# Performance work log

Hardware: AMD Instinct MI355X
Metric: run time of the kernel (lower is better)

The kernel has to match this reference:

```python
import jax, jax.numpy as jnp
import numpy as np
import math

B, T, C, H = 4, 1024, 1024, 16
D = C // H
EPS = 1e-5


def layer_norm(x, w, b):
    mu = jnp.mean(x, axis=-1, keepdims=True)
    var = jnp.mean(jnp.square(x - mu), axis=-1, keepdims=True)
    return (x - mu) * jax.lax.rsqrt(var + EPS) * w + b


def setup_inputs() -> dict:
    key = jax.random.key(0)
    ks = jax.random.split(key, 8)
    s = 0.02
    return {
        "x": jax.random.normal(ks[0], (B, T, C), jnp.float32),
        "attention_mask": jnp.ones((B, T), jnp.float32),
        "ln1_w": jnp.ones((C,), jnp.float32),
        "ln1_b": jnp.zeros((C,), jnp.float32),
        "w_attn": jax.random.normal(ks[1], (C, 3 * C), jnp.float32) * s,
        "b_attn": jnp.zeros((3 * C,), jnp.float32),
        "w_proj": jax.random.normal(ks[2], (C, C), jnp.float32) * s,
        "b_proj": jnp.zeros((C,), jnp.float32),
        "threshold": jnp.float32(0.0005),  # (layer_idx+1)/n_layer * final_token_threshold
        "ln2_w": jnp.ones((C,), jnp.float32),
        "ln2_b": jnp.zeros((C,), jnp.float32),
        "w_fc": jax.random.normal(ks[3], (C, 4 * C), jnp.float32) * s,
        "b_fc": jnp.zeros((4 * C,), jnp.float32),
        "w_fc2": jax.random.normal(ks[4], (4 * C, C), jnp.float32) * s,
        "b_fc2": jnp.zeros((C,), jnp.float32),
    }


def reference(x, attention_mask, ln1_w, ln1_b, w_attn, b_attn, w_proj, b_proj,
              threshold, ln2_w, ln2_b, w_fc, b_fc, w_fc2, b_fc2):
    # ---- attention (eval mode, dropout=0; hard masking_mode) ----
    h = layer_norm(x, ln1_w, ln1_b)
    qkv = h @ w_attn + b_attn                      # (B,T,3C)
    q, k, v = jnp.split(qkv, 3, axis=-1)
    q = q.reshape(B, T, H, D).transpose(0, 2, 1, 3)  # (B,H,T,D)
    k = k.reshape(B, T, H, D).transpose(0, 2, 1, 3)
    v = v.reshape(B, T, H, D).transpose(0, 2, 1, 3)

    scale = 1.0 / math.sqrt(D)
    logits = jnp.einsum("bhqd,bhkd->bhqk", q, k) * scale  # (B,H,T,T)
    causal = jnp.tril(jnp.ones((T, T), bool))
    neg_inf = jnp.float32(-jnp.inf)
    logits = jnp.where(causal[None, None], logits, neg_inf)
    # key-side validity mask (applied in original's manual pass; mask is all-ones
    # here so flash-path y == softmax(causal logits) @ v as well)
    logits = jnp.where(attention_mask[:, None, None, :] == 0, neg_inf, logits)
    att = jax.nn.softmax(logits, axis=-1)

    y = jnp.einsum("bhqk,bhkd->bhqd", att, v)      # (B,H,T,D)
    importance = att.mean(axis=1).mean(axis=1)     # (B,T): mean over heads, then queries

    y = y.transpose(0, 2, 1, 3).reshape(B, T, C)
    x = x + (y @ w_proj + b_proj)

    # ---- hard pruning mask ----
    pruning_mask = (importance >= threshold).astype(x.dtype)
    combined_mask = attention_mask * pruning_mask
    x = x * combined_mask[:, :, None]

    # ---- MLP ----
    h2 = layer_norm(x, ln2_w, ln2_b)
    f = jax.nn.gelu(h2 @ w_fc + b_fc, approximate=False)
    x = x + (f @ w_fc2 + b_fc2)

    pruning_loss = jnp.float32(0.0)  # hard mode -> always 0
    return (x, combined_mask, pruning_loss)
```

## Files before the change

kernel.cpp:

```cpp
#include <hip/hip_runtime.h>
#include <cstdint>
#include <cstring>

typedef unsigned short u16;
typedef short bf16x8 __attribute__((ext_vector_type(8)));
typedef float f32x4 __attribute__((ext_vector_type(4)));

#define MFMA16(a,b,c) __builtin_amdgcn_mfma_f32_16x16x32_bf16(a,b,c,0,0,0)


__device__ __forceinline__ u16 f2bf(float f) {
  union { float f; uint32_t u; } un; un.f = f;
  uint32_t u = un.u;
  u += 0x7FFFu + ((u >> 16) & 1u);
  return (u16)(u >> 16);
}

__device__ __forceinline__ float bf2f(u16 h) {
  union { uint32_t u; float f; } un; un.u = ((uint32_t)h) << 16;
  return un.f;
}

__device__ __forceinline__ float gelu_fast(float v) {
  float u = 0.7978845608028654f * (v + 0.044715f * v * v * v);
  float e = __expf(2.f * u);
  float th = 1.f - __fdividef(2.f, e + 1.f);
  return 0.5f * v * (1.f + th);
}

__device__ __forceinline__ void gl_lds16(const void* g, void* l) {
  __builtin_amdgcn_global_load_lds(
      (__attribute__((address_space(1))) void*)(const_cast<void*>(g)),
      (__attribute__((address_space(3))) void*)l, 16, 0, 0);
}


__global__ __launch_bounds__(256) void transpose_all(
    const float* __restrict__ wa, const float* __restrict__ wp,
    const float* __restrict__ wf, const float* __restrict__ wf2,
    u16* __restrict__ wat, u16* __restrict__ wpt,
    u16* __restrict__ wft, u16* __restrict__ wf2t)
{
  __shared__ float tile[32][33];
  int id = blockIdx.x;
  const float* W; u16* Wt; int K, N, bx, by;
  if (id < 3072)      { W = wa;  Wt = wat;  K = 1024; N = 3072; bx = id % 96;  by = id / 96; }
  else if (id < 4096) { id -= 3072; W = wp;  Wt = wpt;  K = 1024; N = 1024; bx = id % 32; by = id / 32; }
  else if (id < 8192) { id -= 4096; W = wf;  Wt = wft;  K = 1024; N = 4096; bx = id % 128; by = id / 128; }
  else                { id -= 8192; W = wf2; Wt = wf2t; K = 4096; N = 1024; bx = id % 32; by = id / 32; }
  int kt = by * 32, nt = bx * 32;
  int tx = threadIdx.x, ty = threadIdx.y;
#pragma unroll
  for (int i = 0; i < 4; ++i)
    tile[ty + i * 8][tx] = W[(size_t)(kt + ty + i * 8) * N + nt + tx];
  __syncthreads();
#pragma unroll
  for (int i = 0; i < 4; ++i)
    Wt[(size_t)(nt + ty + i * 8) * K + kt + tx] = f2bf(tile[tx][ty + i * 8]);
}


__global__ __launch_bounds__(256) void ln_bf16(
    const float* __restrict__ x, const float* __restrict__ wt,
    const float* __restrict__ bs, u16* __restrict__ out)
{
  int row = blockIdx.x;
  int tid = threadIdx.x, lane = tid & 63, w = tid >> 6;
  const float* xr = x + (size_t)row * 1024;
  float4 v = *(const float4*)(xr + tid * 4);
  float s = v.x + v.y + v.z + v.w;
  float sq = v.x * v.x + v.y * v.y + v.z * v.z + v.w * v.w;
#pragma unroll
  for (int o = 1; o < 64; o <<= 1) { s += __shfl_xor(s, o); sq += __shfl_xor(sq, o); }
  __shared__ float ls[4], lq[4];
  if (lane == 0) { ls[w] = s; lq[w] = sq; }
  __syncthreads();
  s = ls[0] + ls[1] + ls[2] + ls[3];
  sq = lq[0] + lq[1] + lq[2] + lq[3];
  float mu = s * (1.f / 1024.f);
  float var = sq * (1.f / 1024.f) - mu * mu;
  float rstd = rsqrtf(var + 1e-5f);
  float4 wv = *(const float4*)(wt + tid * 4);
  float4 bv = *(const float4*)(bs + tid * 4);
  ushort4 o4;
  o4.x = f2bf((v.x - mu) * rstd * wv.x + bv.x);
  o4.y = f2bf((v.y - mu) * rstd * wv.y + bv.y);
  o4.z = f2bf((v.z - mu) * rstd * wv.z + bv.z);
  o4.w = f2bf((v.w - mu) * rstd * wv.w + bv.w);
  *(ushort4*)(out + (size_t)row * 1024 + tid * 4) = o4;
}


__device__ __forceinline__ void gemm_mainloop_db(
    const u16* __restrict__ Abase, const u16* __restrict__ Bbase,
    int lda, int ldb, int nIter, f32x4 acc[4][4])
{
  __shared__ __align__(16) u16 lA[2][128 * 32];
  __shared__ __align__(16) u16 lB[2][128 * 32];

  const int tid = threadIdx.x;
  const int lane = tid & 63;
  const int w = tid >> 6;
  const int wr = (w >> 1) * 64;
  const int wc = (w & 1) * 64;
  const int laneM = lane & 15;
  const int q4 = lane >> 4;

#pragma unroll
  for (int i = 0; i < 4; ++i)
#pragma unroll
    for (int j = 0; j < 4; ++j)
      acc[i][j] = f32x4{0.f, 0.f, 0.f, 0.f};

  const int off0 = w * 1024 + lane * 16;
  const int off1 = off0 + 4096;
  const int rA0 = off0 >> 6;
  const int rA1 = off1 >> 6;
  const int scb = (((lane & 3) ^ ((lane >> 3) & 3)) << 4);

  const size_t sA = (size_t)lda * 2;
  const size_t sB = (size_t)ldb * 2;
  const char* pA0 = (const char*)Abase + (size_t)rA0 * sA + scb;
  const char* pA1 = (const char*)Abase + (size_t)rA1 * sA + scb;
  const char* pB0 = (const char*)Bbase + (size_t)rA0 * sB + scb;
  const char* pB1 = (const char*)Bbase + (size_t)rA1 * sB + scb;
  char* dA0 = (char*)&lA[0][0] + off0;
  char* dA1 = (char*)&lA[0][0] + off1;
  char* dB0 = (char*)&lB[0][0] + off0;
  char* dB1 = (char*)&lB[0][0] + off1;

  gl_lds16(pA0, dA0); gl_lds16(pA1, dA1);
  gl_lds16(pB0, dB0); gl_lds16(pB1, dB1);
  pA0 += 64; pA1 += 64; pB0 += 64; pB1 += 64;
  __syncthreads();

  const int rdswz = ((q4 ^ ((laneM >> 1) & 3)) << 4);

  for (int it = 0; it < nIter; ++it) {
    const int cur = it & 1;
    const int nb = cur ^ 1;
    if (it + 1 < nIter) {
      gl_lds16(pA0, dA0 + nb * 8192);
      gl_lds16(pA1, dA1 + nb * 8192);
      gl_lds16(pB0, dB0 + nb * 8192);
      gl_lds16(pB1, dB1 + nb * 8192);
      pA0 += 64; pA1 += 64; pB0 += 64; pB1 += 64;
    }
    const char* aRd = (const char*)&lA[cur][0] + (wr + laneM) * 64 + rdswz;
    const char* bRd = (const char*)&lB[cur][0] + (wc + laneM) * 64 + rdswz;
    bf16x8 af[4], bfr[4];
#pragma unroll
    for (int t = 0; t < 4; ++t) {
      af[t]  = *(const bf16x8*)(aRd + t * 1024);
      bfr[t] = *(const bf16x8*)(bRd + t * 1024);
    }
#pragma unroll
    for (int i = 0; i < 4; ++i)
#pragma unroll
      for (int j = 0; j < 4; ++j)
        acc[i][j] = MFMA16(af[i], bfr[j], acc[i][j]);
    if (it + 1 < nIter) __syncthreads();
  }
}


__global__ __launch_bounds__(256, 4) void gemm_qkv(
    const u16* __restrict__ A, const u16* __restrict__ Bt,
    const float* __restrict__ bias,
    u16* __restrict__ qo, u16* __restrict__ ko, u16* __restrict__ vo)
{
  f32x4 acc[4][4];
  int m0 = blockIdx.y * 128, n0 = blockIdx.x * 128;
  gemm_mainloop_db(A + (size_t)m0 * 1024, Bt + (size_t)n0 * 1024, 1024, 1024, 32, acc);
  const int lane = threadIdx.x & 63, w = threadIdx.x >> 6;
  const int wr = (w >> 1) * 64, wc = (w & 1) * 64;
  const int laneM = lane & 15, q4 = lane >> 4;
  const int which = (n0 >> 10);
#pragma unroll
  for (int ti = 0; ti < 4; ++ti) {
#pragma unroll
    for (int tj = 0; tj < 4; ++tj) {
      int n = n0 + wc + tj * 16 + laneM;
      int c = n & 1023;
      int hh = c >> 6, d = c & 63;
      float bval = bias[n];
      if (which == 2) {
        int m0r = m0 + wr + ti * 16 + q4 * 4;
        int b = m0r >> 10, t0 = m0r & 1023;
        ushort4 o4;
        o4.x = f2bf(acc[ti][tj][0] + bval);
        o4.y = f2bf(acc[ti][tj][1] + bval);
        o4.z = f2bf(acc[ti][tj][2] + bval);
        o4.w = f2bf(acc[ti][tj][3] + bval);
        *(ushort4*)&vo[((size_t)((b * 16 + hh) * 64 + d)) * 1024 + t0] = o4;
      } else {
        u16* dst = (which == 0) ? qo : ko;
#pragma unroll
        for (int r = 0; r < 4; ++r) {
          int m = m0 + wr + ti * 16 + q4 * 4 + r;
          int b = m >> 10, t = m & 1023;
          dst[((size_t)((b * 16 + hh) * 1024 + t)) * 64 + d] = f2bf(acc[ti][tj][r] + bval);
        }
      }
    }
  }
}

__global__ __launch_bounds__(256, 4) void gemm_proj(
    const u16* __restrict__ A, const u16* __restrict__ Bt,
    const float* __restrict__ bias, const float* __restrict__ xin,
    const float* __restrict__ maskv, float* __restrict__ x2)
{
  f32x4 acc[4][4];
  int m0 = blockIdx.y * 128, n0 = blockIdx.x * 128;
  gemm_mainloop_db(A + (size_t)m0 * 1024, Bt + (size_t)n0 * 1024, 1024, 1024, 32, acc);
  const int lane = threadIdx.x & 63, w = threadIdx.x >> 6;
  const int wr = (w >> 1) * 64, wc = (w & 1) * 64;
  const int laneM = lane & 15, q4 = lane >> 4;
#pragma unroll
  for (int ti = 0; ti < 4; ++ti) {
#pragma unroll
    for (int tj = 0; tj < 4; ++tj) {
      int n = n0 + wc + tj * 16 + laneM;
      float bval = bias[n];
#pragma unroll
      for (int r = 0; r < 4; ++r) {
        int m = m0 + wr + ti * 16 + q4 * 4 + r;
        float v = xin[(size_t)m * 1024 + n] + acc[ti][tj][r] + bval;
        x2[(size_t)m * 1024 + n] = v * maskv[m];
      }
    }
  }
}

__global__ __launch_bounds__(256, 4) void gemm_fc(
    const u16* __restrict__ A, const u16* __restrict__ Bt,
    const float* __restrict__ bias, u16* __restrict__ fo)
{
  f32x4 acc[4][4];
  int m0 = blockIdx.y * 128, n0 = blockIdx.x * 128;
  gemm_mainloop_db(A + (size_t)m0 * 1024, Bt + (size_t)n0 * 1024, 1024, 1024, 32, acc);
  const int lane = threadIdx.x & 63, w = threadIdx.x >> 6;
  const int wr = (w >> 1) * 64, wc = (w & 1) * 64;
  const int laneM = lane & 15, q4 = lane >> 4;
#pragma unroll
  for (int ti = 0; ti < 4; ++ti) {
#pragma unroll
    for (int tj = 0; tj < 4; ++tj) {
      int n = n0 + wc + tj * 16 + laneM;
      float bval = bias[n];
#pragma unroll
      for (int r = 0; r < 4; ++r) {
        int m = m0 + wr + ti * 16 + q4 * 4 + r;
        fo[(size_t)m * 4096 + n] = f2bf(gelu_fast(acc[ti][tj][r] + bval));
      }
    }
  }
}

__global__ __launch_bounds__(256, 4) void gemm_fc2_splitk(
    const u16* __restrict__ A, const u16* __restrict__ Bt,
    u16* __restrict__ pall)
{
  int id = blockIdx.x;
  int r = id & 7, j = id >> 3;
  int mt = r * 4 + (j >> 5);
  int rem = j & 31;
  int n0 = (rem & 7) * 128;
  int kz = rem >> 3;
  int m0 = mt * 128;
  f32x4 acc[4][4];
  gemm_mainloop_db(A + (size_t)m0 * 4096 + kz * 1024,
                   Bt + (size_t)n0 * 4096 + kz * 1024, 4096, 4096, 32, acc);
  u16* p = pall + (size_t)kz * 4096 * 1024;
  const int lane = threadIdx.x & 63, w = threadIdx.x >> 6;
  const int wr = (w >> 1) * 64, wc = (w & 1) * 64;
  const int laneM = lane & 15, q4 = lane >> 4;
#pragma unroll
  for (int ti = 0; ti < 4; ++ti) {
#pragma unroll
    for (int tj = 0; tj < 4; ++tj) {
      int n = n0 + wc + tj * 16 + laneM;
#pragma unroll
      for (int r2 = 0; r2 < 4; ++r2) {
        int m = m0 + wr + ti * 16 + q4 * 4 + r2;
        p[(size_t)m * 1024 + n] = f2bf(acc[ti][tj][r2]);
      }
    }
  }
}

__global__ __launch_bounds__(256) void fc2_finalize(
    const float* __restrict__ x2, const float* __restrict__ bias,
    const u16* __restrict__ pall, float* __restrict__ out)
{
  int i = blockIdx.x * 256 + threadIdx.x;
  int col4 = i & 255;
  float4 a = ((const float4*)x2)[i];
  float4 b = ((const float4*)bias)[col4];
  float s0 = a.x + b.x, s1 = a.y + b.y, s2 = a.z + b.z, s3 = a.w + b.w;
#pragma unroll
  for (int z = 0; z < 4; ++z) {
    ushort4 u = ((const ushort4*)(pall + (size_t)z * 4194304))[i];
    s0 += bf2f(u.x); s1 += bf2f(u.y); s2 += bf2f(u.z); s3 += bf2f(u.w);
  }
  float4 o; o.x = s0; o.y = s1; o.z = s2; o.w = s3;
  ((float4*)out)[i] = o;
}


__global__ __launch_bounds__(512) void attn_fwd(
    const u16* __restrict__ qb, const u16* __restrict__ kb, const u16* __restrict__ vtb,
    u16* __restrict__ yb, float* __restrict__ part)
{
  const int id = blockIdx.x;
  const int slot = (id & 7) ^ ((id >> 8) & 1);
  const int qbi = (slot & 1) ? (slot >> 1) : (7 - (slot >> 1));
  const int bh = id >> 3;
  const int b = bh >> 4, h = bh & 15;

  const int tid = threadIdx.x, lane = tid & 63, w = tid >> 6;
  const int q0 = qbi * 128;
  const int laneM = lane & 15, q4 = lane >> 4;
  const float scale = 0.125f;

  __shared__ __align__(16) u16 lK[2][64 * 72];
  __shared__ __align__(16) u16 lV[2][64 * 72];
  __shared__ __align__(16) u16 lP[8][16 * 72];
  __shared__ float part_s[1024];

  part_s[tid] = 0.f;
  part_s[tid + 512] = 0.f;

  bf16x8 qf[2];
  {
    const u16* qrow = qb + ((size_t)(bh * 1024 + q0 + w * 16 + laneM)) * 64 + q4 * 8;
    qf[0] = *(const bf16x8*)qrow;
    qf[1] = *(const bf16x8*)(qrow + 32);
  }

  const int nkt = 2 * qbi + 2;
  const int srow = tid >> 3;
  const int scol = (tid & 7) * 8;
  const u16* kbase = kb + (size_t)bh * 65536;
  const u16* vbase = vtb + (size_t)bh * 65536;

  float lrow[4] = {0.f, 0.f, 0.f, 0.f};
  {
    uint4 pk = *(const uint4*)(kbase + (size_t)srow * 64 + scol);
    *(uint4*)&lK[0][srow * 72 + scol] = pk;
    __syncthreads();
    for (int kt = 0; kt < nkt; ++kt) {
      const int cur = kt & 1;
      if (kt + 1 < nkt)
        pk = *(const uint4*)(kbase + (size_t)((kt + 1) * 64 + srow) * 64 + scol);
#pragma unroll
      for (int tj = 0; tj < 4; ++tj) {
        const u16* kp = &lK[cur][(tj * 16 + laneM) * 72 + q4 * 8];
        bf16x8 k0 = *(const bf16x8*)kp;
        bf16x8 k1 = *(const bf16x8*)(kp + 32);
        f32x4 z = {0.f, 0.f, 0.f, 0.f};
        z = MFMA16(qf[0], k0, z);
        z = MFMA16(qf[1], k1, z);
        int kc = kt * 64 + tj * 16 + laneM;
#pragma unroll
        for (int r = 0; r < 4; ++r) {
          int qg = q0 + w * 16 + q4 * 4 + r;
          lrow[r] += (kc <= qg) ? __expf(z[r] * scale) : 0.f;
        }
      }
      if (kt + 1 < nkt) *(uint4*)&lK[cur ^ 1][srow * 72 + scol] = pk;
      __syncthreads();
    }
  }
  float linv[4];
#pragma unroll
  for (int r = 0; r < 4; ++r) {
    float s = lrow[r];
    s += __shfl_xor(s, 1); s += __shfl_xor(s, 2);
    s += __shfl_xor(s, 4); s += __shfl_xor(s, 8);
    linv[r] = 1.f / s;
  }

  f32x4 o_[4];
#pragma unroll
  for (int dt = 0; dt < 4; ++dt) o_[dt] = f32x4{0.f, 0.f, 0.f, 0.f};

  {
    uint4 pk = *(const uint4*)(kbase + (size_t)srow * 64 + scol);
    uint4 pv = *(const uint4*)(vbase + (size_t)srow * 1024 + scol);
    *(uint4*)&lK[0][srow * 72 + scol] = pk;
    *(uint4*)&lV[0][srow * 72 + scol] = pv;
    __syncthreads();
    for (int kt = 0; kt < nkt; ++kt) {
      const int cur = kt & 1;
      if (kt + 1 < nkt) {
        pk = *(const uint4*)(kbase + (size_t)((kt + 1) * 64 + srow) * 64 + scol);
        pv = *(const uint4*)(vbase + (size_t)srow * 1024 + (kt + 1) * 64 + scol);
      }
      u16* lPw = &lP[w][0];
#pragma unroll
      for (int tj = 0; tj < 4; ++tj) {
        const u16* kp = &lK[cur][(tj * 16 + laneM) * 72 + q4 * 8];
        bf16x8 k0 = *(const bf16x8*)kp;
        bf16x8 k1 = *(const bf16x8*)(kp + 32);
        f32x4 z = {0.f, 0.f, 0.f, 0.f};
        z = MFMA16(qf[0], k0, z);
        z = MFMA16(qf[1], k1, z);
        int kc = kt * 64 + tj * 16 + laneM;
        float cs = 0.f;
#pragma unroll
        for (int r = 0; r < 4; ++r) {
          int qg = q0 + w * 16 + q4 * 4 + r;
          float pvf = (kc <= qg) ? __expf(z[r] * scale) * linv[r] : 0.f;
          cs += pvf;
          lPw[(q4 * 4 + r) * 72 + tj * 16 + laneM] = f2bf(pvf);
        }
        cs += __shfl_xor(cs, 16);
        cs += __shfl_xor(cs, 32);
        if (lane < 16) atomicAdd(&part_s[kt * 64 + tj * 16 + lane], cs);
      }
#pragma unroll
      for (int ss = 0; ss < 2; ++ss) {
        bf16x8 pf = *(const bf16x8*)&lP[w][laneM * 72 + ss * 32 + q4 * 8];
#pragma unroll
        for (int dt = 0; dt < 4; ++dt) {
          bf16x8 vf = *(const bf16x8*)&lV[cur][(dt * 16 + laneM) * 72 + ss * 32 + q4 * 8];
          o_[dt] = MFMA16(pf, vf, o_[dt]);
        }
      }
      if (kt + 1 < nkt) {
        *(uint4*)&lK[cur ^ 1][srow * 72 + scol] = pk;
        *(uint4*)&lV[cur ^ 1][srow * 72 + scol] = pv;
      }
      __syncthreads();
    }
  }

  const int kmax = nkt * 64;
  for (int i = tid; i < kmax; i += 512)
    atomicAdd(&part[(size_t)bh * 1024 + i], part_s[i]);

#pragma unroll
  for (int dt = 0; dt < 4; ++dt)
#pragma unroll
    for (int r = 0; r < 4; ++r) {
      int qg = q0 + w * 16 + q4 * 4 + r;
      yb[((size_t)(b * 1024 + qg)) * 1024 + h * 64 + dt * 16 + laneM] = f2bf(o_[dt][r]);
    }
}


__global__ __launch_bounds__(256) void finalize_mask(
    const float* __restrict__ part, const float* __restrict__ amask,
    const float* __restrict__ thr, float* __restrict__ mask_ws,
    float* __restrict__ out_mask, float* __restrict__ out_loss)
{
  int i = blockIdx.x * 256 + threadIdx.x;
  if (i >= 4096) return;
  int b = i >> 10;
  int t = i & 1023;
  float s = 0.f;
#pragma unroll
  for (int hh = 0; hh < 16; ++hh) s += part[(size_t)(b * 16 + hh) * 1024 + t];
  float imp = s * (1.0f / 16384.0f);
  float mv = (imp >= thr[0]) ? amask[i] : 0.f;
  mask_ws[i] = mv;
  out_mask[i] = mv;
  if (i == 0) out_loss[0] = 0.f;
}


extern "C" void kernel_launch(void* const* d_in, const int* in_sizes, int n_in,
                              void* d_out, int out_size, void* d_ws, size_t ws_size,
                              hipStream_t stream) {
  const float* x      = (const float*)d_in[0];
  const float* amask  = (const float*)d_in[1];
  const float* ln1w   = (const float*)d_in[2];
  const float* ln1b   = (const float*)d_in[3];
  const float* w_attn = (const float*)d_in[4];
  const float* b_attn = (const float*)d_in[5];
  const float* w_proj = (const float*)d_in[6];
  const float* b_proj = (const float*)d_in[7];
  const float* thr    = (const float*)d_in[8];
  const float* ln2w   = (const float*)d_in[9];
  const float* ln2b   = (const float*)d_in[10];
  const float* w_fc   = (const float*)d_in[11];
  const float* b_fc   = (const float*)d_in[12];
  const float* w_fc2  = (const float*)d_in[13];
  const float* b_fc2  = (const float*)d_in[14];
  float* out = (float*)d_out;

  char* ws = (char*)d_ws;
  size_t off = 0;
  auto alloc = [&](size_t bytes) -> char* {
    char* p = ws + off;
    off += (bytes + 255) & ~(size_t)255;
    return p;
  };
  u16* wattnT = (u16*)alloc((size_t)3072 * 1024 * 2);
  u16* wprojT = (u16*)alloc((size_t)1024 * 1024 * 2);
  u16* wfcT   = (u16*)alloc((size_t)4096 * 1024 * 2);
  u16* wfc2T  = (u16*)alloc((size_t)1024 * 4096 * 2);
  u16* hbuf   = (u16*)alloc((size_t)4096 * 1024 * 2);
  u16* qbuf   = (u16*)alloc((size_t)64 * 1024 * 64 * 2);
  u16* kbuf   = (u16*)alloc((size_t)64 * 1024 * 64 * 2);
  u16* vtbuf  = (u16*)alloc((size_t)64 * 64 * 1024 * 2);
  u16* ybuf   = (u16*)alloc((size_t)4096 * 1024 * 2);
  float* part = (float*)alloc((size_t)64 * 1024 * 4);
  float* maskws = (float*)alloc((size_t)4096 * 4);
  float* x2   = (float*)alloc((size_t)4096 * 1024 * 4);
  u16* h2     = (u16*)alloc((size_t)4096 * 1024 * 2);
  u16* fbuf   = (u16*)alloc((size_t)4096 * 4096 * 2);

  u16* pall = qbuf;

  transpose_all<<<12288, dim3(32, 8), 0, stream>>>(
      w_attn, w_proj, w_fc, w_fc2, wattnT, wprojT, wfcT, wfc2T);

  hipMemsetAsync(part, 0, (size_t)64 * 1024 * 4, stream);

  ln_bf16<<<4096, 256, 0, stream>>>(x, ln1w, ln1b, hbuf);

  gemm_qkv<<<dim3(24, 32), 256, 0, stream>>>(hbuf, wattnT, b_attn, qbuf, kbuf, vtbuf);

  attn_fwd<<<512, 512, 0, stream>>>(qbuf, kbuf, vtbuf, ybuf, part);

  finalize_mask<<<16, 256, 0, stream>>>(part, amask, thr, maskws,
                                        out + 4194304, out + 4198400);

  gemm_proj<<<dim3(8, 32), 256, 0, stream>>>(ybuf, wprojT, b_proj, x, maskws, x2);

  ln_bf16<<<4096, 256, 0, stream>>>(x2, ln2w, ln2b, h2);

  gemm_fc<<<dim3(32, 32), 256, 0, stream>>>(h2, wfcT, b_fc, fbuf);

  gemm_fc2_splitk<<<1024, 256, 0, stream>>>(fbuf, wfc2T, pall);

  fc2_finalize<<<4096, 256, 0, stream>>>(x2, b_fc2, pall, out);
}
```

Before: 347.1 us.

## Fuse prep, mask finalize, and split-K reduction into neighbouring kernels

Weight transposes and the first LayerNorm now run in one `prep` launch, which also zeroes the split-K tile counters. Attention blocks store their importance partials per query block with plain stores instead of atomics, so the memset of `part` goes away. `gemm_proj` now sums those partials itself to build the pruning mask, removing the `finalize_mask` kernel. The split-K FC2 reduction moves into the last-arriving block per tile via an atomic counter, removing `fc2_finalize`. The aim is fewer launches and less contention on atomics. In exchange, `part` needs eight times more scratch, and each proj block redundantly reads 128 partial values per row.

```diff
diff --git a/kernel.cpp b/kernel.cpp
--- a/kernel.cpp
+++ b/kernel.cpp
@@ -35,28 +35,61 @@
 }
 
 
-__global__ __launch_bounds__(256) void transpose_all(
+__global__ __launch_bounds__(256) void prep(
     const float* __restrict__ wa, const float* __restrict__ wp,
     const float* __restrict__ wf, const float* __restrict__ wf2,
     u16* __restrict__ wat, u16* __restrict__ wpt,
-    u16* __restrict__ wft, u16* __restrict__ wf2t)
+    u16* __restrict__ wft, u16* __restrict__ wf2t,
+    const float* __restrict__ x, const float* __restrict__ ln1w,
+    const float* __restrict__ ln1b, u16* __restrict__ hbuf,
+    unsigned* __restrict__ cnt)
 {
   __shared__ float tile[32][33];
+  __shared__ float ls[4], lq[4];
   int id = blockIdx.x;
-  const float* W; u16* Wt; int K, N, bx, by;
-  if (id < 3072)      { W = wa;  Wt = wat;  K = 1024; N = 3072; bx = id % 96;  by = id / 96; }
-  else if (id < 4096) { id -= 3072; W = wp;  Wt = wpt;  K = 1024; N = 1024; bx = id % 32; by = id / 32; }
-  else if (id < 8192) { id -= 4096; W = wf;  Wt = wft;  K = 1024; N = 4096; bx = id % 128; by = id / 128; }
-  else                { id -= 8192; W = wf2; Wt = wf2t; K = 4096; N = 1024; bx = id % 32; by = id / 32; }
-  int kt = by * 32, nt = bx * 32;
-  int tx = threadIdx.x, ty = threadIdx.y;
-#pragma unroll
-  for (int i = 0; i < 4; ++i)
-    tile[ty + i * 8][tx] = W[(size_t)(kt + ty + i * 8) * N + nt + tx];
-  __syncthreads();
-#pragma unroll
-  for (int i = 0; i < 4; ++i)
-    Wt[(size_t)(nt + ty + i * 8) * K + kt + tx] = f2bf(tile[tx][ty + i * 8]);
+  int tid = threadIdx.x;
+  if (blockIdx.x == 0) cnt[tid] = 0u;
+
+  if (id < 12288) {
+    const float* W; u16* Wt; int K, N, bx, by;
+    if (id < 3072)      { W = wa;  Wt = wat;  K = 1024; N = 3072; bx = id % 96;  by = id / 96; }
+    else if (id < 4096) { id -= 3072; W = wp;  Wt = wpt;  K = 1024; N = 1024; bx = id % 32; by = id / 32; }
+    else if (id < 8192) { id -= 4096; W = wf;  Wt = wft;  K = 1024; N = 4096; bx = id % 128; by = id / 128; }
+    else                { id -= 8192; W = wf2; Wt = wf2t; K = 4096; N = 1024; bx = id % 32; by = id / 32; }
+    int kt = by * 32, nt = bx * 32;
+    int tx = tid & 31, ty = tid >> 5;
+#pragma unroll
+    for (int i = 0; i < 4; ++i)
+      tile[ty + i * 8][tx] = W[(size_t)(kt + ty + i * 8) * N + nt + tx];
+    __syncthreads();
+#pragma unroll
+    for (int i = 0; i < 4; ++i)
+      Wt[(size_t)(nt + ty + i * 8) * K + kt + tx] = f2bf(tile[tx][ty + i * 8]);
+  } else {
+    int row = id - 12288;
+    int lane = tid & 63, w = tid >> 6;
+    const float* xr = x + (size_t)row * 1024;
+    float4 v = *(const float4*)(xr + tid * 4);
+    float s = v.x + v.y + v.z + v.w;
+    float sq = v.x * v.x + v.y * v.y + v.z * v.z + v.w * v.w;
+#pragma unroll
+    for (int o = 1; o < 64; o <<= 1) { s += __shfl_xor(s, o); sq += __shfl_xor(sq, o); }
+    if (lane == 0) { ls[w] = s; lq[w] = sq; }
+    __syncthreads();
+    s = ls[0] + ls[1] + ls[2] + ls[3];
+    sq = lq[0] + lq[1] + lq[2] + lq[3];
+    float mu = s * (1.f / 1024.f);
+    float var = sq * (1.f / 1024.f) - mu * mu;
+    float rstd = rsqrtf(var + 1e-5f);
+    float4 wv = *(const float4*)(ln1w + tid * 4);
+    float4 bv = *(const float4*)(ln1b + tid * 4);
+    ushort4 o4;
+    o4.x = f2bf((v.x - mu) * rstd * wv.x + bv.x);
+    o4.y = f2bf((v.y - mu) * rstd * wv.y + bv.y);
+    o4.z = f2bf((v.z - mu) * rstd * wv.z + bv.z);
+    o4.w = f2bf((v.w - mu) * rstd * wv.w + bv.w);
+    *(ushort4*)(hbuf + (size_t)row * 1024 + tid * 4) = o4;
+  }
 }
 
 
@@ -209,7 +242,53 @@
 __global__ __launch_bounds__(256, 4) void gemm_proj(
     const u16* __restrict__ A, const u16* __restrict__ Bt,
     const float* __restrict__ bias, const float* __restrict__ xin,
-    const float* __restrict__ maskv, float* __restrict__ x2)
+    const float* __restrict__ part, const float* __restrict__ amask,
+    const float* __restrict__ thr, float* __restrict__ x2,
+    float* __restrict__ out_mask, float* __restrict__ out_loss)
+{
+  __shared__ float lmask[128];
+  int m0 = blockIdx.y * 128, n0 = blockIdx.x * 128;
+  int tid = threadIdx.x;
+  if (tid < 128) {
+    int m = m0 + tid;
+    int b = m >> 10, t = m & 1023;
+    const float* pb = part + (size_t)(b * 16) * 1024 + t;
+    float s = 0.f;
+#pragma unroll 4
+    for (int qh = 0; qh < 128; ++qh)
+      s += pb[(size_t)((qh >> 4) * 64 + (qh & 15)) * 1024];
+    float imp = s * (1.0f / 16384.0f);
+    float mv = (imp >= thr[0]) ? amask[m] : 0.f;
+    lmask[tid] = mv;
+    if (n0 == 0) out_mask[m] = mv;
+  }
+  if (n0 == 0 && m0 == 0 && tid == 0) out_loss[0] = 0.f;
+
+  f32x4 acc[4][4];
+  gemm_mainloop_db(A + (size_t)m0 * 1024, Bt + (size_t)n0 * 1024, 1024, 1024, 32, acc);
+  const int lane = threadIdx.x & 63, w = threadIdx.x >> 6;
+  const int wr = (w >> 1) * 64, wc = (w & 1) * 64;
+  const int laneM = lane & 15, q4 = lane >> 4;
+#pragma unroll
+  for (int ti = 0; ti < 4; ++ti) {
+#pragma unroll
+    for (int tj = 0; tj < 4; ++tj) {
+      int n = n0 + wc + tj * 16 + laneM;
+      float bval = bias[n];
+#pragma unroll
+      for (int r = 0; r < 4; ++r) {
+        int lm = wr + ti * 16 + q4 * 4 + r;
+        int m = m0 + lm;
+        float v = xin[(size_t)m * 1024 + n] + acc[ti][tj][r] + bval;
+        x2[(size_t)m * 1024 + n] = v * lmask[lm];
+      }
+    }
+  }
+}
+
+__global__ __launch_bounds__(256, 4) void gemm_fc(
+    const u16* __restrict__ A, const u16* __restrict__ Bt,
+    const float* __restrict__ bias, u16* __restrict__ fo)
 {
   f32x4 acc[4][4];
   int m0 = blockIdx.y * 128, n0 = blockIdx.x * 128;
@@ -226,32 +305,6 @@
 #pragma unroll
       for (int r = 0; r < 4; ++r) {
         int m = m0 + wr + ti * 16 + q4 * 4 + r;
-        float v = xin[(size_t)m * 1024 + n] + acc[ti][tj][r] + bval;
-        x2[(size_t)m * 1024 + n] = v * maskv[m];
-      }
-    }
-  }
-}
-
-__global__ __launch_bounds__(256, 4) void gemm_fc(
-    const u16* __restrict__ A, const u16* __restrict__ Bt,
-    const float* __restrict__ bias, u16* __restrict__ fo)
-{
-  f32x4 acc[4][4];
-  int m0 = blockIdx.y * 128, n0 = blockIdx.x * 128;
-  gemm_mainloop_db(A + (size_t)m0 * 1024, Bt + (size_t)n0 * 1024, 1024, 1024, 32, acc);
-  const int lane = threadIdx.x & 63, w = threadIdx.x >> 6;
-  const int wr = (w >> 1) * 64, wc = (w & 1) * 64;
-  const int laneM = lane & 15, q4 = lane >> 4;
-#pragma unroll
-  for (int ti = 0; ti < 4; ++ti) {
-#pragma unroll
-    for (int tj = 0; tj < 4; ++tj) {
-      int n = n0 + wc + tj * 16 + laneM;
-      float bval = bias[n];
-#pragma unroll
-      for (int r = 0; r < 4; ++r) {
-        int m = m0 + wr + ti * 16 + q4 * 4 + r;
         fo[(size_t)m * 4096 + n] = f2bf(gelu_fast(acc[ti][tj][r] + bval));
       }
     }
@@ -260,7 +313,9 @@
 
 __global__ __launch_bounds__(256, 4) void gemm_fc2_splitk(
     const u16* __restrict__ A, const u16* __restrict__ Bt,
-    u16* __restrict__ pall)
+    u16* __restrict__ pall, const float* __restrict__ x2,
+    const float* __restrict__ bias, float* __restrict__ out,
+    unsigned* __restrict__ cnt)
 {
   int id = blockIdx.x;
   int r = id & 7, j = id >> 3;
@@ -273,7 +328,8 @@
   gemm_mainloop_db(A + (size_t)m0 * 4096 + kz * 1024,
                    Bt + (size_t)n0 * 4096 + kz * 1024, 4096, 4096, 32, acc);
   u16* p = pall + (size_t)kz * 4096 * 1024;
-  const int lane = threadIdx.x & 63, w = threadIdx.x >> 6;
+  const int tid = threadIdx.x;
+  const int lane = tid & 63, w = tid >> 6;
   const int wr = (w >> 1) * 64, wc = (w & 1) * 64;
   const int laneM = lane & 15, q4 = lane >> 4;
 #pragma unroll
@@ -288,24 +344,34 @@
       }
     }
   }
-}
-
-__global__ __launch_bounds__(256) void fc2_finalize(
-    const float* __restrict__ x2, const float* __restrict__ bias,
-    const u16* __restrict__ pall, float* __restrict__ out)
-{
-  int i = blockIdx.x * 256 + threadIdx.x;
-  int col4 = i & 255;
-  float4 a = ((const float4*)x2)[i];
-  float4 b = ((const float4*)bias)[col4];
-  float s0 = a.x + b.x, s1 = a.y + b.y, s2 = a.z + b.z, s3 = a.w + b.w;
-#pragma unroll
-  for (int z = 0; z < 4; ++z) {
-    ushort4 u = ((const ushort4*)(pall + (size_t)z * 4194304))[i];
-    s0 += bf2f(u.x); s1 += bf2f(u.y); s2 += bf2f(u.z); s3 += bf2f(u.w);
-  }
-  float4 o; o.x = s0; o.y = s1; o.z = s2; o.w = s3;
-  ((float4*)out)[i] = o;
+
+  __shared__ unsigned done;
+  __syncthreads();
+  const int tile = mt * 8 + (n0 >> 7);
+  if (tid == 0) {
+    __threadfence();
+    done = atomicAdd(&cnt[tile], 1u);
+  }
+  __syncthreads();
+  if (done == 3u) {
+    __threadfence();
+#pragma unroll
+    for (int k = 0; k < 16; ++k) {
+      int idx = k * 256 + tid;
+      int rr = idx >> 5, c = idx & 31;
+      size_t row = (size_t)(m0 + rr);
+      float4 a = ((const float4*)(x2 + row * 1024 + n0))[c];
+      float4 b = ((const float4*)(bias + n0))[c];
+      float s0 = a.x + b.x, s1 = a.y + b.y, s2 = a.z + b.z, s3 = a.w + b.w;
+#pragma unroll
+      for (int z = 0; z < 4; ++z) {
+        ushort4 u = ((const ushort4*)(pall + (size_t)z * 4194304 + row * 1024 + n0))[c];
+        s0 += bf2f(u.x); s1 += bf2f(u.y); s2 += bf2f(u.z); s3 += bf2f(u.w);
+      }
+      float4 o; o.x = s0; o.y = s1; o.z = s2; o.w = s3;
+      ((float4*)(out + row * 1024 + n0))[c] = o;
+    }
+  }
 }
 
 
@@ -437,9 +503,11 @@
     }
   }
 
-  const int kmax = nkt * 64;
-  for (int i = tid; i < kmax; i += 512)
-    atomicAdd(&part[(size_t)bh * 1024 + i], part_s[i]);
+  {
+    float* pd = part + (size_t)(qbi * 64 + bh) * 1024;
+    pd[tid] = part_s[tid];
+    pd[tid + 512] = part_s[tid + 512];
+  }
 
 #pragma unroll
   for (int dt = 0; dt < 4; ++dt)
@@ -448,26 +516,6 @@
       int qg = q0 + w * 16 + q4 * 4 + r;
       yb[((size_t)(b * 1024 + qg)) * 1024 + h * 64 + dt * 16 + laneM] = f2bf(o_[dt][r]);
     }
-}
-
-
-__global__ __launch_bounds__(256) void finalize_mask(
-    const float* __restrict__ part, const float* __restrict__ amask,
-    const float* __restrict__ thr, float* __restrict__ mask_ws,
-    float* __restrict__ out_mask, float* __restrict__ out_loss)
-{
-  int i = blockIdx.x * 256 + threadIdx.x;
-  if (i >= 4096) return;
-  int b = i >> 10;
-  int t = i & 1023;
-  float s = 0.f;
-#pragma unroll
-  for (int hh = 0; hh < 16; ++hh) s += part[(size_t)(b * 16 + hh) * 1024 + t];
-  float imp = s * (1.0f / 16384.0f);
-  float mv = (imp >= thr[0]) ? amask[i] : 0.f;
-  mask_ws[i] = mv;
-  out_mask[i] = mv;
-  if (i == 0) out_loss[0] = 0.f;
 }
 
 
@@ -507,35 +555,28 @@
   u16* kbuf   = (u16*)alloc((size_t)64 * 1024 * 64 * 2);
   u16* vtbuf  = (u16*)alloc((size_t)64 * 64 * 1024 * 2);
   u16* ybuf   = (u16*)alloc((size_t)4096 * 1024 * 2);
-  float* part = (float*)alloc((size_t)64 * 1024 * 4);
-  float* maskws = (float*)alloc((size_t)4096 * 4);
+  float* part = (float*)alloc((size_t)8 * 64 * 1024 * 4);
+  unsigned* cnt = (unsigned*)alloc((size_t)256 * 4);
   float* x2   = (float*)alloc((size_t)4096 * 1024 * 4);
   u16* h2     = (u16*)alloc((size_t)4096 * 1024 * 2);
   u16* fbuf   = (u16*)alloc((size_t)4096 * 4096 * 2);
 
   u16* pall = qbuf;
 
-  transpose_all<<<12288, dim3(32, 8), 0, stream>>>(
-      w_attn, w_proj, w_fc, w_fc2, wattnT, wprojT, wfcT, wfc2T);
-
-  hipMemsetAsync(part, 0, (size_t)64 * 1024 * 4, stream);
-
-  ln_bf16<<<4096, 256, 0, stream>>>(x, ln1w, ln1b, hbuf);
+  prep<<<16384, 256, 0, stream>>>(w_attn, w_proj, w_fc, w_fc2,
+                                  wattnT, wprojT, wfcT, wfc2T,
+                                  x, ln1w, ln1b, hbuf, cnt);
 
   gemm_qkv<<<dim3(24, 32), 256, 0, stream>>>(hbuf, wattnT, b_attn, qbuf, kbuf, vtbuf);
 
   attn_fwd<<<512, 512, 0, stream>>>(qbuf, kbuf, vtbuf, ybuf, part);
 
-  finalize_mask<<<16, 256, 0, stream>>>(part, amask, thr, maskws,
-                                        out + 4194304, out + 4198400);
-
-  gemm_proj<<<dim3(8, 32), 256, 0, stream>>>(ybuf, wprojT, b_proj, x, maskws, x2);
+  gemm_proj<<<dim3(8, 32), 256, 0, stream>>>(ybuf, wprojT, b_proj, x, part, amask,
+                                             thr, x2, out + 4194304, out + 4198400);
 
   ln_bf16<<<4096, 256, 0, stream>>>(x2, ln2w, ln2b, h2);
 
   gemm_fc<<<dim3(32, 32), 256, 0, stream>>>(h2, wfcT, b_fc, fbuf);
 
-  gemm_fc2_splitk<<<1024, 256, 0, stream>>>(fbuf, wfc2T, pall);
-
-  fc2_finalize<<<4096, 256, 0, stream>>>(x2, b_fc2, pall, out);
-}
+  gemm_fc2_splitk<<<1024, 256, 0, stream>>>(fbuf, wfc2T, pall, x2, b_fc2, out, cnt);
+}
```

Result: slower. 446.0 us (+28.5%).

## Use 64x64 vectorized transpose tiles and raise wave priority around attention MFMAs

Applied to the files above, without the earlier changes.

The weight transpose/convert kernel now works on 64x64 tiles with float4 loads and ushort4 stores instead of 32x32 scalar accesses, cutting the block count and the number of memory transactions. The attention kernel also wraps its MFMA sequences in s_setprio so waves issuing matrix ops get scheduling priority over waves doing exp and softmax work. The larger LDS tile lowers occupancy for the transpose. Its column reads of the padded tile may also hit bank conflicts.

```diff
diff --git a/kernel.cpp b/kernel.cpp
--- a/kernel.cpp
+++ b/kernel.cpp
@@ -41,22 +41,36 @@
     u16* __restrict__ wat, u16* __restrict__ wpt,
     u16* __restrict__ wft, u16* __restrict__ wf2t)
 {
-  __shared__ float tile[32][33];
+  __shared__ float tile[64][65];
   int id = blockIdx.x;
   const float* W; u16* Wt; int K, N, bx, by;
-  if (id < 3072)      { W = wa;  Wt = wat;  K = 1024; N = 3072; bx = id % 96;  by = id / 96; }
-  else if (id < 4096) { id -= 3072; W = wp;  Wt = wpt;  K = 1024; N = 1024; bx = id % 32; by = id / 32; }
-  else if (id < 8192) { id -= 4096; W = wf;  Wt = wft;  K = 1024; N = 4096; bx = id % 128; by = id / 128; }
-  else                { id -= 8192; W = wf2; Wt = wf2t; K = 4096; N = 1024; bx = id % 32; by = id / 32; }
-  int kt = by * 32, nt = bx * 32;
-  int tx = threadIdx.x, ty = threadIdx.y;
-#pragma unroll
-  for (int i = 0; i < 4; ++i)
-    tile[ty + i * 8][tx] = W[(size_t)(kt + ty + i * 8) * N + nt + tx];
+  if (id < 768)       { W = wa;  Wt = wat;  K = 1024; N = 3072; bx = id % 48; by = id / 48; }
+  else if (id < 1024) { id -= 768;  W = wp;  Wt = wpt;  K = 1024; N = 1024; bx = id % 16; by = id / 16; }
+  else if (id < 2048) { id -= 1024; W = wf;  Wt = wft;  K = 1024; N = 4096; bx = id % 64; by = id / 64; }
+  else                { id -= 2048; W = wf2; Wt = wf2t; K = 4096; N = 1024; bx = id % 16; by = id / 16; }
+  int kt = by * 64, nt = bx * 64;
+  int tid = threadIdx.x;
+  int tx = tid & 15, ty = tid >> 4;
+#pragma unroll
+  for (int i = 0; i < 4; ++i) {
+    int r = ty + i * 16;
+    float4 v = *(const float4*)&W[(size_t)(kt + r) * N + nt + tx * 4];
+    tile[r][tx * 4 + 0] = v.x;
+    tile[r][tx * 4 + 1] = v.y;
+    tile[r][tx * 4 + 2] = v.z;
+    tile[r][tx * 4 + 3] = v.w;
+  }
   __syncthreads();
 #pragma unroll
-  for (int i = 0; i < 4; ++i)
-    Wt[(size_t)(nt + ty + i * 8) * K + kt + tx] = f2bf(tile[tx][ty + i * 8]);
+  for (int i = 0; i < 4; ++i) {
+    int n = ty + i * 16;
+    ushort4 o4;
+    o4.x = f2bf(tile[tx * 4 + 0][n]);
+    o4.y = f2bf(tile[tx * 4 + 1][n]);
+    o4.z = f2bf(tile[tx * 4 + 2][n]);
+    o4.w = f2bf(tile[tx * 4 + 3][n]);
+    *(ushort4*)&Wt[(size_t)(nt + n) * K + kt + tx * 4] = o4;
+  }
 }
 
 
@@ -360,8 +374,10 @@
         bf16x8 k0 = *(const bf16x8*)kp;
         bf16x8 k1 = *(const bf16x8*)(kp + 32);
         f32x4 z = {0.f, 0.f, 0.f, 0.f};
+        __builtin_amdgcn_s_setprio(1);
         z = MFMA16(qf[0], k0, z);
         z = MFMA16(qf[1], k1, z);
+        __builtin_amdgcn_s_setprio(0);
         int kc = kt * 64 + tj * 16 + laneM;
 #pragma unroll
         for (int r = 0; r < 4; ++r) {
@@ -405,8 +421,10 @@
         bf16x8 k0 = *(const bf16x8*)kp;
         bf16x8 k1 = *(const bf16x8*)(kp + 32);
         f32x4 z = {0.f, 0.f, 0.f, 0.f};
+        __builtin_amdgcn_s_setprio(1);
         z = MFMA16(qf[0], k0, z);
         z = MFMA16(qf[1], k1, z);
+        __builtin_amdgcn_s_setprio(0);
         int kc = kt * 64 + tj * 16 + laneM;
         float cs = 0.f;
 #pragma unroll
@@ -420,6 +438,7 @@
         cs += __shfl_xor(cs, 32);
         if (lane < 16) atomicAdd(&part_s[kt * 64 + tj * 16 + lane], cs);
       }
+      __builtin_amdgcn_s_setprio(1);
 #pragma unroll
       for (int ss = 0; ss < 2; ++ss) {
         bf16x8 pf = *(const bf16x8*)&lP[w][laneM * 72 + ss * 32 + q4 * 8];
@@ -429,6 +448,7 @@
           o_[dt] = MFMA16(pf, vf, o_[dt]);
         }
       }
+      __builtin_amdgcn_s_setprio(0);
       if (kt + 1 < nkt) {
         *(uint4*)&lK[cur ^ 1][srow * 72 + scol] = pk;
         *(uint4*)&lV[cur ^ 1][srow * 72 + scol] = pv;
@@ -515,7 +535,7 @@
 
   u16* pall = qbuf;
 
-  transpose_all<<<12288, dim3(32, 8), 0, stream>>>(
+  transpose_all<<<3072, 256, 0, stream>>>(
       w_attn, w_proj, w_fc, w_fc2, wattnT, wprojT, wfcT, wfc2T);
 
   hipMemsetAsync(part, 0, (size_t)64 * 1024 * 4, stream);
```

New measurement: 346.6 us. About the same (-0.1%).
